# Optimization experiments

Hardware: AMD Instinct MI355X
Metric: run time of the kernel (lower is better)

Reference implementation:

```python
import jax, jax.numpy as jnp
import numpy as np

EPS = 1e-5
GROUPS = 8


def conv3x3(x, w, b):
    # x: [B,Cin,H,W], w: [Cout,Cin,3,3]
    y = jax.lax.conv_general_dilated(x, w, (1, 1), 'SAME',
                                     dimension_numbers=('NCHW', 'OIHW', 'NCHW'))
    return y + b[None, :, None, None]


def group_norm(x, scale, bias):
    B, C, H, W = x.shape
    xg = x.reshape(B, GROUPS, C // GROUPS, H, W)
    mu = jnp.mean(xg, axis=(2, 3, 4), keepdims=True)
    var = jnp.var(xg, axis=(2, 3, 4), keepdims=True)
    xn = ((xg - mu) * jax.lax.rsqrt(var + EPS)).reshape(B, C, H, W)
    return xn * scale[None, :, None, None] + bias[None, :, None, None]


def setup_inputs() -> dict:
    key = jax.random.key(0)
    ks = jax.random.split(key, 18)
    B, C, D, H, W = 8, 256, 128, 128, 128
    s = 0.02
    return {
        'current_feat': jax.random.normal(ks[0], (B, C, H, W), jnp.float32),
        'prev_hidden': jax.random.normal(ks[1], (B, D, H, W), jnp.float32),
        'conv1_w': jax.random.normal(ks[2], (D, C, 3, 3), jnp.float32) * s,
        'conv1_b': jnp.zeros((D,), jnp.float32),
        'gn_scale': jnp.ones((D,), jnp.float32),
        'gn_bias': jnp.zeros((D,), jnp.float32),
        'ce_w1': jax.random.normal(ks[3], (64, 4), jnp.float32) * 0.5,
        'ce_b1': jnp.zeros((64,), jnp.float32),
        'ce_w2': jax.random.normal(ks[4], (D, 64), jnp.float32) * 0.125,
        'ce_b2': jnp.zeros((D,), jnp.float32),
        'w_ih': jax.random.normal(ks[5], (3 * D, 3 * D), jnp.float32) * s,
        'b_ih': jnp.zeros((3 * D,), jnp.float32),
        'w_hh': jax.random.normal(ks[6], (3 * D, D), jnp.float32) * s,
        'b_hh': jnp.zeros((3 * D,), jnp.float32),
        'conv2_w': jax.random.normal(ks[7], (C, D, 3, 3), jnp.float32) * s,
        'conv2_b': jnp.zeros((C,), jnp.float32),
    }


def reference(current_feat, prev_hidden, conv1_w, conv1_b, gn_scale, gn_bias,
              ce_w1, ce_b1, ce_w2, ce_b2, w_ih, b_ih, w_hh, b_hh,
              conv2_w, conv2_b):
    B, C, H, W = current_feat.shape
    D = conv1_w.shape[0]

    # spatial_proj: conv -> GroupNorm(8) -> exact GELU
    spatial = jax.nn.gelu(group_norm(conv3x3(current_feat, conv1_w, conv1_b),
                                     gn_scale, gn_bias), approximate=False)

    # coordinate embedding (Linear(4,64) -> ReLU -> Linear(64,D))
    xc = jnp.broadcast_to(jnp.linspace(-1.0, 1.0, W)[None, None, :], (B, H, W))
    yc = jnp.broadcast_to(jnp.linspace(-1.0, 1.0, H)[None, :, None], (B, H, W))
    coord = jnp.stack([xc, yc, xc * H, yc * W], axis=-1)       # [B,H,W,4]
    ce = jax.nn.relu(coord @ ce_w1.T + ce_b1) @ ce_w2.T + ce_b2  # [B,H,W,D]
    coord_emb = jnp.transpose(ce, (0, 3, 1, 2))                 # [B,D,H,W]

    # batched GRUCell over all B*H*W positions (no spatial recurrence)
    gru_in = jnp.concatenate([spatial, coord_emb, prev_hidden], axis=1)  # [B,3D,H,W]
    Xf = jnp.transpose(gru_in, (0, 2, 3, 1)).reshape(-1, 3 * D)          # [N,3D]
    hf = jnp.transpose(prev_hidden, (0, 2, 3, 1)).reshape(-1, D)         # [N,D]
    gi = Xf @ w_ih.T + b_ih
    gh = hf @ w_hh.T + b_hh
    i_r, i_z, i_n = jnp.split(gi, 3, axis=-1)
    h_r, h_z, h_n = jnp.split(gh, 3, axis=-1)
    r = jax.nn.sigmoid(i_r + h_r)
    z = jax.nn.sigmoid(i_z + h_z)
    n = jnp.tanh(i_n + r * h_n)
    h_new = (1.0 - z) * n + z * hf                                       # [N,D]
    new_hidden = jnp.transpose(h_new.reshape(B, H, W, D), (0, 3, 1, 2))  # [B,D,H,W]

    # output_proj (Dropout2d inactive in eval) + residual
    output_feat = conv3x3(new_hidden, conv2_w, conv2_b) + current_feat
    return output_feat, new_hidden
```

## Files before the change

kernel.cpp:

```cpp
#include <hip/hip_runtime.h>
#include <math.h>

#define BH 8
#define HH 128
#define WW 128
#define HW 16384

typedef __attribute__((ext_vector_type(8))) short bf16x8;
typedef __attribute__((ext_vector_type(4))) float f32x4;

__device__ inline unsigned short f2bf(float f) {
    union { float f; unsigned u; } v; v.f = f;
    unsigned r = v.u + 0x7FFF + ((v.u >> 16) & 1);
    return (unsigned short)(r >> 16);
}
__device__ inline float bf2f(unsigned short u) {
    union { unsigned u; float f; } v; v.u = (unsigned)u << 16;
    return v.f;
}

__global__ __launch_bounds__(256) void transpose_cast(
        const float* __restrict__ in, unsigned short* __restrict__ out, int C) {
    __shared__ float T[32][65];
    int tid = threadIdx.x;
    int pb = blockIdx.x * 64, cb = blockIdx.y * 32, b = blockIdx.z;
    #pragma unroll
    for (int j = 0; j < 8; ++j) {
        int idx = tid + j * 256;
        int c = idx >> 6, p = idx & 63;
        T[c][p] = in[((size_t)(b * C + cb + c)) * HW + pb + p];
    }
    __syncthreads();
    #pragma unroll
    for (int j = 0; j < 8; ++j) {
        int idx = tid + j * 256;
        int p = idx >> 5, c = idx & 31;
        out[((size_t)(b * HW + pb + p)) * C + cb + c] = f2bf(T[c][p]);
    }
}

__global__ __launch_bounds__(256) void repack_weights(
        const float* __restrict__ w1, const float* __restrict__ w2,
        const float* __restrict__ wih, const float* __restrict__ whh,
        unsigned short* __restrict__ w1t, unsigned short* __restrict__ w2t,
        unsigned short* __restrict__ wg) {
    int i = blockIdx.x * 256 + threadIdx.x;
    if (i < 294912) {
        int t = i >> 15, rem = i & 32767, d = rem >> 8, c = rem & 255;
        w1t[i] = f2bf(w1[((size_t)(d * 256 + c)) * 9 + t]);
    }
    if (i < 294912) {
        int t = i >> 15, co = (i >> 7) & 255, ci = i & 127;
        w2t[i] = f2bf(w2[((size_t)(co * 128 + ci)) * 9 + t]);
    }
    if (i < 196608) {
        int m = i / 384, k = i - m * 384;
        float v = 0.0f;
        if (m < 384) {
            if (k < 128)       v = wih[(size_t)m * 384 + k];
            else if (k < 256)  v = wih[(size_t)m * 384 + 256 + (k - 128)];
            else               v = (m < 256) ? whh[(size_t)m * 128 + (k - 256)] : 0.0f;
        } else {
            v = (k >= 256) ? whh[(size_t)(m - 128) * 128 + (k - 256)] : 0.0f;
        }
        wg[i] = f2bf(v);
    }
}

__global__ __launch_bounds__(256) void prep_ce(
        const float* __restrict__ w2, const float* __restrict__ b2,
        const float* __restrict__ wih,
        float* __restrict__ M, float* __restrict__ cebias) {
    int i = blockIdx.x * 256 + threadIdx.x;
    if (i < 24576) {
        int j = i / 384, m = i - j * 384;
        float acc = 0.0f;
        for (int d = 0; d < 128; ++d)
            acc = fmaf(w2[(size_t)d * 64 + j], wih[(size_t)m * 384 + 128 + d], acc);
        M[i] = acc;
    } else if (i < 24960) {
        int m = i - 24576;
        float acc = 0.0f;
        for (int d = 0; d < 128; ++d)
            acc = fmaf(b2[d], wih[(size_t)m * 384 + 128 + d], acc);
        cebias[m] = acc;
    }
}

__global__ __launch_bounds__(384) void ce_g_kernel(
        const float* __restrict__ w1, const float* __restrict__ b1,
        const float* __restrict__ M, const float* __restrict__ cebias,
        float* __restrict__ ce_g) {
    __shared__ float h1[16][64];
    int m = threadIdx.x;
    int pos0 = blockIdx.x * 16;
    for (int e = m; e < 1024; e += 384) {
        int p = e >> 6, j = e & 63;
        int pos = pos0 + p;
        int hh = pos >> 7, wp = pos & 127;
        float xc = -1.0f + 2.0f * (float)wp / 127.0f;
        float yc = -1.0f + 2.0f * (float)hh / 127.0f;
        float a = xc * w1[j*4+0] + yc * w1[j*4+1]
                + xc * 128.0f * w1[j*4+2] + yc * 128.0f * w1[j*4+3] + b1[j];
        h1[p][j] = fmaxf(a, 0.0f);
    }
    __syncthreads();
    float acc[16];
    float cb = cebias[m];
    #pragma unroll
    for (int p = 0; p < 16; ++p) acc[p] = cb;
    for (int j = 0; j < 64; ++j) {
        float Mv = M[(size_t)j * 384 + m];
        #pragma unroll
        for (int p = 0; p < 16; ++p)
            acc[p] = fmaf(h1[p][j], Mv, acc[p]);
    }
    #pragma unroll
    for (int p = 0; p < 16; ++p)
        ce_g[(size_t)(pos0 + p) * 384 + m] = acc[p];
}

template<int CIN, int COUT, bool CONV1>
__global__ __launch_bounds__(256) void conv_mfma(
        const unsigned short* __restrict__ xt,
        const unsigned short* __restrict__ wt,
        const float* __restrict__ bias,
        float* __restrict__ stats_acc,
        const float* __restrict__ resid,
        unsigned short* __restrict__ y_bf,
        float* __restrict__ y_f32) {
    __shared__ unsigned short Ash[130 * 40];
    __shared__ unsigned short Wsh[3 * 128 * 40];

    const int tid = threadIdx.x;
    const int h = blockIdx.x, b = blockIdx.y;
    const int cobase = blockIdx.z * 128;
    const int lane = tid & 63, wave = tid >> 6;
    const int wn = (wave & 1) * 64, wd = (wave >> 1) * 64;
    const int l15 = lane & 15, quad = lane >> 4;
    const int kb = quad * 8;

    f32x4 acc[4][4];
    #pragma unroll
    for (int i = 0; i < 4; ++i)
        #pragma unroll
        for (int j = 0; j < 4; ++j)
            acc[i][j] = (f32x4){0.f, 0.f, 0.f, 0.f};

    for (int kh = 0; kh < 3; ++kh) {
        int r = h + kh - 1;
        if (r < 0 || r >= HH) continue;
        const unsigned short* xrow = xt + ((size_t)(b * HW + r * WW)) * CIN;
        for (int cc = 0; cc < CIN / 32; ++cc) {
            int c0 = cc * 32;
            __syncthreads();
            #pragma unroll
            for (int j = 0; j < 9; ++j) {
                int idx = tid + j * 256;
                if (idx < 2080) {
                    int i = idx >> 4, cp = (idx & 15) * 2;
                    unsigned int val = 0;
                    if (i >= 1 && i <= 128)
                        val = *(const unsigned int*)(xrow + (size_t)(i - 1) * CIN + c0 + cp);
                    *(unsigned int*)&Ash[i * 40 + cp] = val;
                }
            }
            #pragma unroll
            for (int j = 0; j < 12; ++j) {
                int idx = tid + j * 256;
                int kw = idx >> 10;
                int rem = idx & 1023;
                int d = rem >> 3, kq = (rem & 7) * 4;
                int t = kh * 3 + kw;
                const unsigned short* wp =
                    wt + ((size_t)t * COUT + cobase + d) * CIN + c0 + kq;
                *(ushort4*)&Wsh[(kw * 128 + d) * 40 + kq] = *(const ushort4*)wp;
            }
            __syncthreads();
            #pragma unroll
            for (int kw = 0; kw < 3; ++kw) {
                bf16x8 a[4], bb[4];
                #pragma unroll
                for (int fn = 0; fn < 4; ++fn)
                    a[fn] = *(const bf16x8*)&Ash[(wn + fn * 16 + l15 + kw) * 40 + kb];
                #pragma unroll
                for (int fd = 0; fd < 4; ++fd)
                    bb[fd] = *(const bf16x8*)&Wsh[(kw * 128 + wd + fd * 16 + l15) * 40 + kb];
                #pragma unroll
                for (int fn = 0; fn < 4; ++fn)
                    #pragma unroll
                    for (int fd = 0; fd < 4; ++fd)
                        acc[fn][fd] = __builtin_amdgcn_mfma_f32_16x16x32_bf16(
                            a[fn], bb[fd], acc[fn][fd], 0, 0, 0);
            }
        }
    }

    if (CONV1) {
        float gsum[4] = {0.f,0.f,0.f,0.f}, gss[4] = {0.f,0.f,0.f,0.f};
        #pragma unroll
        for (int fd = 0; fd < 4; ++fd) {
            int d = wd + fd * 16 + l15;
            float bv = bias[d];
            #pragma unroll
            for (int fn = 0; fn < 4; ++fn) {
                #pragma unroll
                for (int reg = 0; reg < 4; ++reg) {
                    int n = wn + fn * 16 + quad * 4 + reg;
                    float v = acc[fn][fd][reg] + bv;
                    y_bf[((size_t)(b * HW + h * WW + n)) * 128 + d] = f2bf(v);
                    gsum[fd] += v; gss[fd] += v * v;
                }
            }
        }
        #pragma unroll
        for (int fd = 0; fd < 4; ++fd) {
            float s = gsum[fd], q = gss[fd];
            for (int o = 32; o > 0; o >>= 1) {
                s += __shfl_down(s, o);
                q += __shfl_down(q, o);
            }
            if (lane == 0) {
                int g = (wd >> 4) + fd;
                atomicAdd(&stats_acc[(b * 8 + g) * 2], s);
                atomicAdd(&stats_acc[(b * 8 + g) * 2 + 1], q);
            }
        }
    } else {
        #pragma unroll
        for (int fd = 0; fd < 4; ++fd) {
            int co = cobase + wd + fd * 16 + l15;
            float bv = bias[co];
            #pragma unroll
            for (int fn = 0; fn < 4; ++fn) {
                int n0 = wn + fn * 16 + quad * 4;
                size_t ofs = ((size_t)(b * 256 + co)) * HW + h * WW + n0;
                float4 rs = *(const float4*)(resid + ofs);
                float4 o;
                o.x = acc[fn][fd][0] + bv + rs.x;
                o.y = acc[fn][fd][1] + bv + rs.y;
                o.z = acc[fn][fd][2] + bv + rs.z;
                o.w = acc[fn][fd][3] + bv + rs.w;
                *(float4*)(y_f32 + ofs) = o;
            }
        }
    }
}

__global__ void gn_finalize(float* stats) {
    int t = threadIdx.x;
    if (t < 64) {
        float s = stats[t*2], q = stats[t*2+1];
        const float inv = 1.0f / 262144.0f;
        float mean = s * inv;
        float var = q * inv - mean * mean;
        stats[t*2] = mean;
        stats[t*2+1] = rsqrtf(var + 1e-5f);
    }
}

__global__ __launch_bounds__(256) void gn_gelu(
        unsigned short* __restrict__ y, const float* __restrict__ stats,
        const float* __restrict__ scale, const float* __restrict__ bias) {
    size_t i = (size_t)blockIdx.x * 256 + threadIdx.x;
    size_t e = i * 4;
    int d = (int)(e & 127);
    int b = (int)(e >> 21);
    int g = b * 8 + (d >> 4);
    float mean = stats[g * 2], rstd = stats[g * 2 + 1];
    ushort4 v = *(ushort4*)&y[e];
    unsigned short vs[4] = {v.x, v.y, v.z, v.w};
    #pragma unroll
    for (int j = 0; j < 4; ++j) {
        float a = rstd * scale[d + j];
        float c = bias[d + j] - mean * a;
        float t = bf2f(vs[j]) * a + c;
        vs[j] = f2bf(0.5f * t * (1.0f + erff(t * 0.70710678118654752f)));
    }
    ushort4 o = {vs[0], vs[1], vs[2], vs[3]};
    *(ushort4*)&y[e] = o;
}

__global__ __launch_bounds__(256) void gru_gemm(
        const unsigned short* __restrict__ sp_t,
        const unsigned short* __restrict__ ph_t,
        const unsigned short* __restrict__ wg,
        unsigned short* __restrict__ G) {
    __shared__ unsigned short Xs[128 * 40];
    __shared__ unsigned short Wgs[128 * 40];
    const int tid = threadIdx.x;
    const int nt = blockIdx.x, mt = blockIdx.y;
    const size_t p0 = (size_t)nt * 128;
    const int lane = tid & 63, wave = tid >> 6;
    const int wn = (wave & 1) * 64, wm = (wave >> 1) * 64;
    const int l15 = lane & 15, quad = lane >> 4, kb = quad * 8;

    f32x4 acc[4][4];
    #pragma unroll
    for (int i = 0; i < 4; ++i)
        #pragma unroll
        for (int j = 0; j < 4; ++j)
            acc[i][j] = (f32x4){0.f, 0.f, 0.f, 0.f};

    for (int ck = 0; ck < 12; ++ck) {
        int k0 = ck * 32;
        const unsigned short* xsrc;
        if (k0 < 128)      xsrc = sp_t + p0 * 128 + k0;
        else if (k0 < 256) xsrc = ph_t + p0 * 128 + (k0 - 128);
        else               xsrc = ph_t + p0 * 128 + (k0 - 256);
        __syncthreads();
        #pragma unroll
        for (int j = 0; j < 4; ++j) {
            int idx = tid + j * 256;
            int n = idx >> 3, kq = (idx & 7) * 4;
            *(ushort4*)&Xs[n * 40 + kq] = *(const ushort4*)(xsrc + (size_t)n * 128 + kq);
        }
        #pragma unroll
        for (int j = 0; j < 4; ++j) {
            int idx = tid + j * 256;
            int m = idx >> 3, kq = (idx & 7) * 4;
            *(ushort4*)&Wgs[m * 40 + kq] =
                *(const ushort4*)(wg + ((size_t)(mt * 128 + m)) * 384 + k0 + kq);
        }
        __syncthreads();
        bf16x8 a[4], bb[4];
        #pragma unroll
        for (int fn = 0; fn < 4; ++fn)
            a[fn] = *(const bf16x8*)&Xs[(wn + fn * 16 + l15) * 40 + kb];
        #pragma unroll
        for (int fm = 0; fm < 4; ++fm)
            bb[fm] = *(const bf16x8*)&Wgs[(wm + fm * 16 + l15) * 40 + kb];
        #pragma unroll
        for (int fn = 0; fn < 4; ++fn)
            #pragma unroll
            for (int fm = 0; fm < 4; ++fm)
                acc[fn][fm] = __builtin_amdgcn_mfma_f32_16x16x32_bf16(
                    a[fn], bb[fm], acc[fn][fm], 0, 0, 0);
    }
    #pragma unroll
    for (int fm = 0; fm < 4; ++fm) {
        int m = mt * 128 + wm + fm * 16 + l15;
        #pragma unroll
        for (int fn = 0; fn < 4; ++fn)
            #pragma unroll
            for (int reg = 0; reg < 4; ++reg) {
                int n = wn + fn * 16 + quad * 4 + reg;
                G[(p0 + n) * 512 + m] = f2bf(acc[fn][fm][reg]);
            }
    }
}

__global__ __launch_bounds__(256) void gru_gate(
        const unsigned short* __restrict__ G,
        const float* __restrict__ ce_g,
        const float* __restrict__ b_ih, const float* __restrict__ b_hh,
        const float* __restrict__ prev_f32,
        float* __restrict__ new_hidden, unsigned short* __restrict__ hn_t) {
    __shared__ float T[128][65];
    const int tid = threadIdx.x;
    const size_t p0 = (size_t)blockIdx.x * 64;
    const int b = (int)(p0 >> 14);
    const int hw0 = (int)(p0 & (HW - 1));
    const int d = tid & 127;
    const float br  = b_ih[d]       + b_hh[d];
    const float bz  = b_ih[128 + d] + b_hh[128 + d];
    const float bin = b_ih[256 + d];
    const float bhn = b_hh[256 + d];
    for (int j = 0; j < 32; ++j) {
        int pp = (tid >> 7) + j * 2;
        size_t gbase = (p0 + pp) * 512;
        size_t cbase = (size_t)(hw0 + pp) * 384;
        float rl = bf2f(G[gbase + d])       + ce_g[cbase + d]       + br;
        float zl = bf2f(G[gbase + 128 + d]) + ce_g[cbase + 128 + d] + bz;
        float il = bf2f(G[gbase + 256 + d]) + ce_g[cbase + 256 + d] + bin;
        float hl = bf2f(G[gbase + 384 + d]) + bhn;
        float r = 1.0f / (1.0f + expf(-rl));
        float z = 1.0f / (1.0f + expf(-zl));
        float n = tanhf(il + r * hl);
        float hp = prev_f32[((size_t)(b * 128 + d)) * HW + hw0 + pp];
        float hn = (1.0f - z) * n + z * hp;
        T[d][pp] = hn;
        hn_t[(p0 + pp) * 128 + d] = f2bf(hn);
    }
    __syncthreads();
    #pragma unroll
    for (int j = 0; j < 8; ++j) {
        int idx = tid + j * 256;
        int d2 = idx >> 4, pp4 = (idx & 15) * 4;
        float4 v = { T[d2][pp4], T[d2][pp4+1], T[d2][pp4+2], T[d2][pp4+3] };
        *(float4*)&new_hidden[((size_t)(b * 128 + d2)) * HW + hw0 + pp4] = v;
    }
}

extern "C" void kernel_launch(void* const* d_in, const int* in_sizes, int n_in,
                              void* d_out, int out_size, void* d_ws, size_t ws_size,
                              hipStream_t stream) {
    const float* current_feat = (const float*)d_in[0];
    const float* prev_hidden  = (const float*)d_in[1];
    const float* conv1_w = (const float*)d_in[2];
    const float* conv1_b = (const float*)d_in[3];
    const float* gn_scale = (const float*)d_in[4];
    const float* gn_bias  = (const float*)d_in[5];
    const float* ce_w1 = (const float*)d_in[6];
    const float* ce_b1 = (const float*)d_in[7];
    const float* ce_w2 = (const float*)d_in[8];
    const float* ce_b2 = (const float*)d_in[9];
    const float* w_ih = (const float*)d_in[10];
    const float* b_ih = (const float*)d_in[11];
    const float* w_hh = (const float*)d_in[12];
    const float* b_hh = (const float*)d_in[13];
    const float* conv2_w = (const float*)d_in[14];
    const float* conv2_b = (const float*)d_in[15];

    char* ws = (char*)d_ws;
    unsigned short* cf_t = (unsigned short*)(ws);
    unsigned short* ph_t = (unsigned short*)(ws + 67108864);
    unsigned short* sp_t = (unsigned short*)(ws + 100663296);
    unsigned short* w1t  = (unsigned short*)(ws + 134217728);
    unsigned short* w2t  = (unsigned short*)(ws + 134807552);
    unsigned short* wg   = (unsigned short*)(ws + 135397376);
    float* Mmat          = (float*)(ws + 135790592);
    float* cebias        = (float*)(ws + 135888896);
    float* stats         = (float*)(ws + 135890432);
    unsigned short* hn_t = cf_t;
    float* ce_g          = (float*)(ws + 33554432);
    unsigned short* G    = (unsigned short*)d_out;
    float* out_feat      = (float*)d_out;
    float* new_hidden    = (float*)d_out + 33554432;

    hipMemsetAsync(stats, 0, 512, stream);
    hipLaunchKernelGGL(repack_weights, dim3(1152), dim3(256), 0, stream,
                       conv1_w, conv2_w, w_ih, w_hh, w1t, w2t, wg);
    hipLaunchKernelGGL(prep_ce, dim3(98), dim3(256), 0, stream,
                       ce_w2, ce_b2, w_ih, Mmat, cebias);
    hipLaunchKernelGGL(transpose_cast, dim3(256, 8, 8), dim3(256), 0, stream,
                       current_feat, cf_t, 256);
    hipLaunchKernelGGL(transpose_cast, dim3(256, 4, 8), dim3(256), 0, stream,
                       prev_hidden, ph_t, 128);
    hipLaunchKernelGGL((conv_mfma<256, 128, true>), dim3(128, 8, 1), dim3(256), 0, stream,
                       cf_t, w1t, conv1_b, stats, nullptr, sp_t, nullptr);
    hipLaunchKernelGGL(ce_g_kernel, dim3(1024), dim3(384), 0, stream,
                       ce_w1, ce_b1, Mmat, cebias, ce_g);
    hipLaunchKernelGGL(gn_finalize, dim3(1), dim3(64), 0, stream, stats);
    hipLaunchKernelGGL(gn_gelu, dim3(16384), dim3(256), 0, stream,
                       sp_t, stats, gn_scale, gn_bias);
    hipLaunchKernelGGL(gru_gemm, dim3(1024, 4), dim3(256), 0, stream,
                       sp_t, ph_t, wg, G);
    hipLaunchKernelGGL(gru_gate, dim3(2048), dim3(256), 0, stream,
                       G, ce_g, b_ih, b_hh, prev_hidden, new_hidden, hn_t);
    hipLaunchKernelGGL((conv_mfma<128, 256, false>), dim3(128, 8, 2), dim3(256), 0, stream,
                       hn_t, w2t, conv2_b, nullptr, current_feat, nullptr, out_feat);
}
```

Before: 1.120 ms.

## Double-buffer conv and GRU GEMM tiles with direct global-to-LDS async loads

The conv and GRU GEMM kernels now stage their input and weight tiles into double-buffered shared memory using global_load_lds 16-byte direct loads, so the next K-chunk is fetched while MFMAs run on the current one. The padded LDS layout is replaced by an XOR swizzle to avoid bank conflicts, and a zero buffer supplies out-of-range conv rows so no branch is needed. This roughly doubles LDS use per block and adds occupancy hints. It also depends on the exact per-wave placement semantics of the direct-to-LDS loads being correct.

```diff
diff --git a/kernel.cpp b/kernel.cpp
--- a/kernel.cpp
+++ b/kernel.cpp
@@ -17,6 +17,12 @@
 __device__ inline float bf2f(unsigned short u) {
     union { unsigned u; float f; } v; v.u = (unsigned)u << 16;
     return v.f;
+}
+
+typedef const __attribute__((address_space(1))) void* gptr_t;
+typedef __attribute__((address_space(3))) void* lptr_t;
+__device__ inline void gload_lds16(const void* g, void* l) {
+    __builtin_amdgcn_global_load_lds((gptr_t)g, (lptr_t)l, 16, 0, 0);
 }
 
 __global__ __launch_bounds__(256) void transpose_cast(
@@ -121,16 +127,19 @@
 }
 
 template<int CIN, int COUT, bool CONV1>
-__global__ __launch_bounds__(256) void conv_mfma(
+__global__ __launch_bounds__(256, 2) void conv_mfma(
         const unsigned short* __restrict__ xt,
         const unsigned short* __restrict__ wt,
         const float* __restrict__ bias,
         float* __restrict__ stats_acc,
         const float* __restrict__ resid,
         unsigned short* __restrict__ y_bf,
-        float* __restrict__ y_f32) {
-    __shared__ unsigned short Ash[130 * 40];
-    __shared__ unsigned short Wsh[3 * 128 * 40];
+        float* __restrict__ y_f32,
+        const unsigned short* __restrict__ zbuf) {
+    constexpr int NCC = CIN / 32;
+    constexpr int NT  = 3 * NCC;
+    __shared__ unsigned short Ash[2][130 * 32];
+    __shared__ unsigned short Wsh[2][384 * 32];
 
     const int tid = threadIdx.x;
     const int h = blockIdx.x, b = blockIdx.y;
@@ -138,7 +147,6 @@
     const int lane = tid & 63, wave = tid >> 6;
     const int wn = (wave & 1) * 64, wd = (wave >> 1) * 64;
     const int l15 = lane & 15, quad = lane >> 4;
-    const int kb = quad * 8;
 
     f32x4 acc[4][4];
     #pragma unroll
@@ -147,53 +155,69 @@
         for (int j = 0; j < 4; ++j)
             acc[i][j] = (f32x4){0.f, 0.f, 0.f, 0.f};
 
-    for (int kh = 0; kh < 3; ++kh) {
-        int r = h + kh - 1;
-        if (r < 0 || r >= HH) continue;
-        const unsigned short* xrow = xt + ((size_t)(b * HW + r * WW)) * CIN;
-        for (int cc = 0; cc < CIN / 32; ++cc) {
-            int c0 = cc * 32;
-            __syncthreads();
-            #pragma unroll
-            for (int j = 0; j < 9; ++j) {
-                int idx = tid + j * 256;
-                if (idx < 2080) {
-                    int i = idx >> 4, cp = (idx & 15) * 2;
-                    unsigned int val = 0;
-                    if (i >= 1 && i <= 128)
-                        val = *(const unsigned int*)(xrow + (size_t)(i - 1) * CIN + c0 + cp);
-                    *(unsigned int*)&Ash[i * 40 + cp] = val;
-                }
-            }
-            #pragma unroll
-            for (int j = 0; j < 12; ++j) {
-                int idx = tid + j * 256;
-                int kw = idx >> 10;
-                int rem = idx & 1023;
-                int d = rem >> 3, kq = (rem & 7) * 4;
-                int t = kh * 3 + kw;
-                const unsigned short* wp =
-                    wt + ((size_t)t * COUT + cobase + d) * CIN + c0 + kq;
-                *(ushort4*)&Wsh[(kw * 128 + d) * 40 + kq] = *(const ushort4*)wp;
-            }
-            __syncthreads();
-            #pragma unroll
-            for (int kw = 0; kw < 3; ++kw) {
-                bf16x8 a[4], bb[4];
-                #pragma unroll
-                for (int fn = 0; fn < 4; ++fn)
-                    a[fn] = *(const bf16x8*)&Ash[(wn + fn * 16 + l15 + kw) * 40 + kb];
+    auto stage = [&](int buf, int t) {
+        const int kh = t / NCC, cc = t - kh * NCC;
+        const int r = h + kh - 1;
+        const bool oob = ((unsigned)r >= (unsigned)HH);
+        const char* abase = oob ? (const char*)zbuf
+            : (const char*)(xt + ((size_t)(b * HW + r * WW)) * CIN + cc * 32);
+        #pragma unroll
+        for (int j = 0; j < 2; ++j) {
+            const int ob = 64 + (tid + j * 256) * 16;
+            const int row = ob >> 6, cb = ob & 63;
+            const int sel = (row >> 1) & 3;
+            const char* src = oob ? abase + cb
+                : abase + (size_t)(row - 1) * (CIN * 2) + (cb ^ (sel << 4));
+            gload_lds16(src, (char*)Ash[buf] + 64 + (wave * 64 + j * 256) * 16);
+        }
+        #pragma unroll
+        for (int j = 0; j < 6; ++j) {
+            const int ob = (tid + j * 256) * 16;
+            const int m = ob >> 6, cb = ob & 63;
+            const int sel = (m >> 1) & 3;
+            const int kw = m >> 7, d = m & 127;
+            const char* src = (const char*)wt
+                + (((size_t)(kh * 3 + kw) * COUT + cobase + d) * CIN + cc * 32) * 2
+                + (cb ^ (sel << 4));
+            gload_lds16(src, (char*)Wsh[buf] + (wave * 64 + j * 256) * 16);
+        }
+    };
+
+    if (tid < 16) {
+        int buf = tid >> 3, hi = (tid >> 2) & 1, q = tid & 3;
+        *(f32x4*)((char*)Ash[buf] + (hi ? 129 * 64 : 0) + q * 16) =
+            (f32x4){0.f, 0.f, 0.f, 0.f};
+    }
+    stage(0, 0);
+    __syncthreads();
+
+    int curb = 0;
+    for (int t = 0; t < NT; ++t) {
+        if (t + 1 < NT) stage(curb ^ 1, t + 1);
+        #pragma unroll
+        for (int kw = 0; kw < 3; ++kw) {
+            bf16x8 a[4], bb[4];
+            #pragma unroll
+            for (int fn = 0; fn < 4; ++fn) {
+                int ra = wn + fn * 16 + l15 + kw;
+                a[fn] = *(const bf16x8*)&Ash[curb][ra * 32 +
+                            (quad * 8 ^ (((ra >> 1) & 3) << 3))];
+            }
+            #pragma unroll
+            for (int fd = 0; fd < 4; ++fd) {
+                int m = kw * 128 + wd + fd * 16 + l15;
+                bb[fd] = *(const bf16x8*)&Wsh[curb][m * 32 +
+                            (quad * 8 ^ (((m >> 1) & 3) << 3))];
+            }
+            #pragma unroll
+            for (int fn = 0; fn < 4; ++fn)
                 #pragma unroll
                 for (int fd = 0; fd < 4; ++fd)
-                    bb[fd] = *(const bf16x8*)&Wsh[(kw * 128 + wd + fd * 16 + l15) * 40 + kb];
-                #pragma unroll
-                for (int fn = 0; fn < 4; ++fn)
-                    #pragma unroll
-                    for (int fd = 0; fd < 4; ++fd)
-                        acc[fn][fd] = __builtin_amdgcn_mfma_f32_16x16x32_bf16(
-                            a[fn], bb[fd], acc[fn][fd], 0, 0, 0);
-            }
-        }
+                    acc[fn][fd] = __builtin_amdgcn_mfma_f32_16x16x32_bf16(
+                        a[fn], bb[fd], acc[fn][fd], 0, 0, 0);
+        }
+        __syncthreads();
+        curb ^= 1;
     }
 
     if (CONV1) {
@@ -281,19 +305,19 @@
     *(ushort4*)&y[e] = o;
 }
 
-__global__ __launch_bounds__(256) void gru_gemm(
+__global__ __launch_bounds__(256, 2) void gru_gemm(
         const unsigned short* __restrict__ sp_t,
         const unsigned short* __restrict__ ph_t,
         const unsigned short* __restrict__ wg,
         unsigned short* __restrict__ G) {
-    __shared__ unsigned short Xs[128 * 40];
-    __shared__ unsigned short Wgs[128 * 40];
+    __shared__ unsigned short Xs[2][128 * 32];
+    __shared__ unsigned short Wgs[2][128 * 32];
     const int tid = threadIdx.x;
     const int nt = blockIdx.x, mt = blockIdx.y;
     const size_t p0 = (size_t)nt * 128;
     const int lane = tid & 63, wave = tid >> 6;
     const int wn = (wave & 1) * 64, wm = (wave >> 1) * 64;
-    const int l15 = lane & 15, quad = lane >> 4, kb = quad * 8;
+    const int l15 = lane & 15, quad = lane >> 4;
 
     f32x4 acc[4][4];
     #pragma unroll
@@ -302,40 +326,57 @@
         for (int j = 0; j < 4; ++j)
             acc[i][j] = (f32x4){0.f, 0.f, 0.f, 0.f};
 
+    auto stage = [&](int buf, int ck) {
+        const int k0 = ck * 32;
+        const char* xb = (const char*)((k0 < 128)
+            ? sp_t + p0 * 128 + k0
+            : ph_t + p0 * 128 + (k0 & 127));
+        #pragma unroll
+        for (int j = 0; j < 2; ++j) {
+            const int ob = (tid + j * 256) * 16;
+            const int row = ob >> 6, cb = ob & 63;
+            const int sel = (row >> 1) & 3;
+            gload_lds16(xb + (size_t)row * 256 + (cb ^ (sel << 4)),
+                        (char*)Xs[buf] + (wave * 64 + j * 256) * 16);
+        }
+        #pragma unroll
+        for (int j = 0; j < 2; ++j) {
+            const int ob = (tid + j * 256) * 16;
+            const int row = ob >> 6, cb = ob & 63;
+            const int sel = (row >> 1) & 3;
+            gload_lds16((const char*)wg +
+                            ((size_t)(mt * 128 + row) * 384 + k0) * 2 +
+                            (cb ^ (sel << 4)),
+                        (char*)Wgs[buf] + (wave * 64 + j * 256) * 16);
+        }
+    };
+
+    stage(0, 0);
+    __syncthreads();
+    int curb = 0;
     for (int ck = 0; ck < 12; ++ck) {
-        int k0 = ck * 32;
-        const unsigned short* xsrc;
-        if (k0 < 128)      xsrc = sp_t + p0 * 128 + k0;
-        else if (k0 < 256) xsrc = ph_t + p0 * 128 + (k0 - 128);
-        else               xsrc = ph_t + p0 * 128 + (k0 - 256);
-        __syncthreads();
-        #pragma unroll
-        for (int j = 0; j < 4; ++j) {
-            int idx = tid + j * 256;
-            int n = idx >> 3, kq = (idx & 7) * 4;
-            *(ushort4*)&Xs[n * 40 + kq] = *(const ushort4*)(xsrc + (size_t)n * 128 + kq);
-        }
-        #pragma unroll
-        for (int j = 0; j < 4; ++j) {
-            int idx = tid + j * 256;
-            int m = idx >> 3, kq = (idx & 7) * 4;
-            *(ushort4*)&Wgs[m * 40 + kq] =
-                *(const ushort4*)(wg + ((size_t)(mt * 128 + m)) * 384 + k0 + kq);
-        }
-        __syncthreads();
+        if (ck + 1 < 12) stage(curb ^ 1, ck + 1);
         bf16x8 a[4], bb[4];
         #pragma unroll
-        for (int fn = 0; fn < 4; ++fn)
-            a[fn] = *(const bf16x8*)&Xs[(wn + fn * 16 + l15) * 40 + kb];
-        #pragma unroll
-        for (int fm = 0; fm < 4; ++fm)
-            bb[fm] = *(const bf16x8*)&Wgs[(wm + fm * 16 + l15) * 40 + kb];
+        for (int fn = 0; fn < 4; ++fn) {
+            int row = wn + fn * 16 + l15;
+            a[fn] = *(const bf16x8*)&Xs[curb][row * 32 +
+                        (quad * 8 ^ (((row >> 1) & 3) << 3))];
+        }
+        #pragma unroll
+        for (int fm = 0; fm < 4; ++fm) {
+            int row = wm + fm * 16 + l15;
+            bb[fm] = *(const bf16x8*)&Wgs[curb][row * 32 +
+                        (quad * 8 ^ (((row >> 1) & 3) << 3))];
+        }
         #pragma unroll
         for (int fn = 0; fn < 4; ++fn)
             #pragma unroll
             for (int fm = 0; fm < 4; ++fm)
                 acc[fn][fm] = __builtin_amdgcn_mfma_f32_16x16x32_bf16(
                     a[fn], bb[fm], acc[fn][fm], 0, 0, 0);
+        __syncthreads();
+        curb ^= 1;
     }
     #pragma unroll
     for (int fm = 0; fm < 4; ++fm) {
@@ -422,6 +463,7 @@
     float* Mmat          = (float*)(ws + 135790592);
     float* cebias        = (float*)(ws + 135888896);
     float* stats         = (float*)(ws + 135890432);
+    unsigned short* zbuf = (unsigned short*)(ws + 135890944);
     unsigned short* hn_t = cf_t;
     float* ce_g          = (float*)(ws + 33554432);
     unsigned short* G    = (unsigned short*)d_out;
@@ -429,6 +471,7 @@
     float* new_hidden    = (float*)d_out + 33554432;
 
     hipMemsetAsync(stats, 0, 512, stream);
+    hipMemsetAsync(zbuf, 0, 256, stream);
     hipLaunchKernelGGL(repack_weights, dim3(1152), dim3(256), 0, stream,
                        conv1_w, conv2_w, w_ih, w_hh, w1t, w2t, wg);
     hipLaunchKernelGGL(prep_ce, dim3(98), dim3(256), 0, stream,
@@ -438,7 +481,7 @@
     hipLaunchKernelGGL(transpose_cast, dim3(256, 4, 8), dim3(256), 0, stream,
                        prev_hidden, ph_t, 128);
     hipLaunchKernelGGL((conv_mfma<256, 128, true>), dim3(128, 8, 1), dim3(256), 0, stream,
-                       cf_t, w1t, conv1_b, stats, nullptr, sp_t, nullptr);
+                       cf_t, w1t, conv1_b, stats, nullptr, sp_t, nullptr, zbuf);
     hipLaunchKernelGGL(ce_g_kernel, dim3(1024), dim3(384), 0, stream,
                        ce_w1, ce_b1, Mmat, cebias, ce_g);
     hipLaunchKernelGGL(gn_finalize, dim3(1), dim3(64), 0, stream, stats);
@@ -449,5 +492,5 @@
     hipLaunchKernelGGL(gru_gate, dim3(2048), dim3(256), 0, stream,
                        G, ce_g, b_ih, b_hh, prev_hidden, new_hidden, hn_t);
     hipLaunchKernelGGL((conv_mfma<128, 256, false>), dim3(128, 8, 2), dim3(256), 0, stream,
-                       hn_t, w2t, conv2_b, nullptr, current_feat, nullptr, out_feat);
-}
+                       hn_t, w2t, conv2_b, nullptr, current_feat, nullptr, out_feat, zbuf);
+}
```

After: 1.039 ms. 1.08x faster.
